# Kernel optimization log

Hardware: AMD Instinct MI355X
Metric: run time of the kernel (lower is better)

## Reference

```python
import jax, jax.numpy as jnp
import numpy as np

LMAX = 2
L = LMAX + 1          # number of l channels
M = (LMAX + 1) ** 2   # 9 spherical components
C = 64                # channels per l
N = 1024              # nodes
E = 300               # num_elements (hard-coded in module)
P3, P2, P1 = 16, 4, 2 # CG path counts for correlation 3/2/1


def so3_linear(x, w, b=None):
    # x: [N, M, Cin]; w: [L, Cout, Cin]. Per-l channel mixing (equivariant),
    # bias only on the l=0 (scalar) block.
    outs = []
    for l in range(L):
        seg = x[:, l * l:(l + 1) * (l + 1), :]
        y = jnp.einsum('nmc,dc->nmd', seg, w[l])
        if l == 0 and b is not None:
            y = y + b
        outs.append(y)
    return jnp.concatenate(outs, axis=1)


def setup_inputs() -> dict:
    key = jax.random.key(0)
    ks = jax.random.split(key, 13)
    s = lambda k, shape, sc=1.0: jax.random.normal(k, shape, dtype=jnp.float32) * sc
    return {
        'irreps_x': s(ks[0], (N, M, C)),
        'atomic_numbers': jax.random.randint(ks[1], (N,), 0, 119),
        'w_fc1': s(ks[2], (L, C, C), 1.0 / np.sqrt(C)),
        'b_fc1': jnp.zeros((C,), jnp.float32),
        'U3': s(ks[3], (M, M, M, M, P3), 0.05),   # generalized CG coeffs, corr 3
        'W3': s(ks[4], (E, P3, C), 1.0 / np.sqrt(P3 * C)),
        'U2': s(ks[5], (M, M, M, P2), 0.05),      # corr 2
        'W2': s(ks[6], (E, P2, C), 1.0 / np.sqrt(P2 * C)),
        'U1': s(ks[7], (M, M, P1), 0.05),         # corr 1
        'W1': s(ks[8], (E, P1, C), 1.0 / np.sqrt(P1 * C)),
        'w_lin': s(ks[9], (L, C, C), 1.0 / np.sqrt(C)),   # e3nn Linear in dtp block
        'w_fc2': s(ks[10], (L, C, C), 1.0 / np.sqrt(C)),  # final SO3_Linear
        'b_fc2': jnp.zeros((C,), jnp.float32),
    }


def reference(irreps_x, atomic_numbers, w_fc1, b_fc1, U3, W3, U2, W2, U1, W1,
              w_lin, w_fc2, b_fc2):
    # 1) irreps_small_fc
    x = so3_linear(irreps_x, w_fc1, b_fc1)           # [N, M, C]
    # 2) permute(0, 2, 1): MACE layout [N, C, M]
    xT = jnp.transpose(x, (0, 2, 1))
    # one_hot(atomic_numbers) @ W  ==  gather of per-element weights
    a = atomic_numbers.astype(jnp.int32)
    w3 = W3[a]                                        # [N, P3, C]
    w2 = W2[a]                                        # [N, P2, C]
    w1 = W1[a]                                        # [N, P1, C]
    # MACE symmetric contraction, correlation = 3:
    # out[n,c,o,a,b] = sum_{i,p} U3[o,a,b,i,p] * w3[n,p,c] * x[n,c,i]
    z = jnp.einsum('nci,npc->ncip', xT, w3)           # [N, C, M, P3]
    out = jnp.einsum('oabip,ncip->ncoab', U3, z)      # [N, C, M, M, M]
    # fold in correlation-2 term, contract one input index
    c2 = jnp.einsum('oaip,npc->ncoai', U2, w2)        # [N, C, M, M, M]
    out = jnp.einsum('ncoai,nci->ncoa', c2 + out, xT) # [N, C, M, M]
    # fold in correlation-1 term, contract last input index
    c1 = jnp.einsum('oip,npc->ncoi', U1, w1)          # [N, C, M, M]
    out = jnp.einsum('ncoi,nci->nco', c1 + out, xT)   # [N, C, M]
    # e3nn per-irrep Linear inside EquivariantProductBasisBlock (no bias)
    out = jnp.transpose(out, (0, 2, 1))               # back2orderTmul -> [N, M, C]
    out = so3_linear(out, w_lin)
    # 3) final SO3_Linear back to input channel count
    out = so3_linear(out, w_fc2, b_fc2)
    return out                                        # [N, M, C]
```

## Files before the change

### kernel.cpp

```cpp
#include <hip/hip_runtime.h>


typedef __attribute__((ext_vector_type(8)))  _Float16 f16x8;
typedef __attribute__((ext_vector_type(4)))  _Float16 f16x4;
typedef __attribute__((ext_vector_type(16))) float    f32x16;
typedef __attribute__((ext_vector_type(4)))  float    f32x4;
typedef __attribute__((ext_vector_type(8)))  short    short8;

static __device__ __forceinline__ unsigned short f2bf(float f) {
    union { float f; unsigned u; } v; v.f = f;
    unsigned r = v.u + 0x7fffu + ((v.u >> 16) & 1u);
    return (unsigned short)(r >> 16);
}

__global__ void prep_u3w(const float* __restrict__ U3, const float* __restrict__ U2,
                         _Float16* __restrict__ U3w)
{
    int idx = blockIdx.x * 256 + threadIdx.x;
    int ks = idx / 192, r = idx % 192;
    int nt = r >> 6, l = r & 63;
    int oa = nt * 32 + (l & 31), half = l >> 5;
    f16x8 v;
    if (ks < 81) {
        int b = ks / 9, ksub = ks % 9, ip0 = ksub * 16 + half * 8;
        #pragma unroll
        for (int j = 0; j < 8; ++j) {
            float f = (oa < 81) ? U3[(oa * 9 + b) * 144 + ip0 + j] : 0.f;
            v[j] = (_Float16)f;
        }
    } else {
        int ip0 = (ks - 81) * 16 + half * 8;
        #pragma unroll
        for (int j = 0; j < 8; ++j) {
            int ip2 = ip0 + j;
            float f = (oa < 81 && ip2 < 36) ? U2[oa * 36 + ip2] : 0.f;
            v[j] = (_Float16)f;
        }
    }
    ((f16x8*)U3w)[idx] = v;
}

__global__ __launch_bounds__(384, 3) void mace_main(
    const float* __restrict__ irreps_x,
    const int*   __restrict__ atomic_numbers,
    const float* __restrict__ w_fc1,
    const float* __restrict__ b_fc1,
    const float* __restrict__ W3,
    const float* __restrict__ W2,
    const float* __restrict__ U1,
    const float* __restrict__ W1,
    const float* __restrict__ w_lin,
    const float* __restrict__ w_fc2,
    const float* __restrict__ b_fc2,
    const _Float16* __restrict__ U3w,
    float* __restrict__ out)
{
    __shared__ float xvL[1152];
    __shared__ __align__(16) unsigned char region[47616];
    _Float16* const o2L       = (_Float16*)region;
    float* const o1L          = (float*)region;
    unsigned short* const XfA = (unsigned short*)(region + 4608);
    unsigned short* const WfA = (unsigned short*)(region + 17408);
    float* const yL           = (float*)(region + 43008);

    const int t  = threadIdx.x;
    const int n0 = blockIdx.x * 2;
    const int w  = t >> 6;
    const int l  = t & 63;
    const int kg = l >> 4;
    const int hf = l >> 5;
    const int c32 = l & 31;

    auto fill_Xf = [&](auto srcf) {
        for (int i = t; i < 32 * 96; i += 384) {
            int rr = i / 96, k = (i % 96) * 2;
            int lh = k >> 6, c = k & 63;
            float v0 = 0.f, v1 = 0.f;
            if (rr < 18) {
                int at = rr / 9, m = rr % 9;
                int lm = (m >= 4) ? 2 : (m >= 1 ? 1 : 0);
                if (lh == lm) { v0 = srcf(at, m, c); v1 = srcf(at, m, c + 1); }
            }
            unsigned pk = (unsigned)f2bf(v0) | ((unsigned)f2bf(v1) << 16);
            *(unsigned*)(XfA + rr * 200 + k) = pk;
        }
    };
    auto fill_Wf = [&](const float* wmat) {
        for (int i = t; i < 64 * 96; i += 384) {
            int d = i / 96, k = (i % 96) * 2;
            int lh = k >> 6, c = k & 63;
            const float* wp = wmat + lh * 4096 + d * 64 + c;
            unsigned pk = (unsigned)f2bf(wp[0]) | ((unsigned)f2bf(wp[1]) << 16);
            *(unsigned*)(WfA + d * 200 + k) = pk;
        }
    };
    auto run_linear = [&](const float* bias, float* dst, bool to_global) {
        for (int tile = w; tile < 8; tile += 6) {
            int rt = tile >> 2, ct = tile & 3;
            int row = rt * 16 + (l & 15);
            int col = ct * 16 + (l & 15);
            const unsigned short* ab = XfA + row * 200 + kg * 8;
            const unsigned short* bb = WfA + col * 200 + kg * 8;
            f32x4 acc0 = {0,0,0,0}, acc1 = {0,0,0,0};
            #pragma unroll
            for (int kt = 0; kt < 6; kt += 2) {
                short8 A0 = *(const short8*)(ab + kt * 32);
                short8 A1 = *(const short8*)(ab + (kt + 1) * 32);
                short8 B0 = *(const short8*)(bb + kt * 32);
                short8 B1 = *(const short8*)(bb + (kt + 1) * 32);
                acc0 = __builtin_amdgcn_mfma_f32_16x16x32_bf16(A0, B0, acc0, 0, 0, 0);
                acc1 = __builtin_amdgcn_mfma_f32_16x16x32_bf16(A1, B1, acc1, 0, 0, 0);
            }
            f32x4 acc = acc0 + acc1;
            #pragma unroll
            for (int r = 0; r < 4; ++r) {
                int rr = rt * 16 + kg * 4 + r;
                if (rr < 18) {
                    int at = rr / 9, m = rr % 9;
                    float v = acc[r];
                    if (bias && m == 0) v += bias[col];
                    if (to_global) dst[(n0 + at) * 576 + m * 64 + col] = v;
                    else           dst[at * 576 + m * 64 + col] = v;
                }
            }
        }
    };

    fill_Xf([&](int at, int m, int c) { return irreps_x[(n0 + at) * 576 + m * 64 + c]; });
    fill_Wf(w_fc1);
    __syncthreads();
    run_linear(b_fc1, xvL, false);
    __syncthreads();

    {
        const int at = w / 3, ng = w % 3;
        const int an = atomic_numbers[n0 + at];
        const float* xa  = xvL + at * 576;
        const float* W3r = W3 + an * 1024;
        const float* W2r = W2 + an * 256;

        f16x8 s3f[2][9];
        #pragma unroll
        for (int mt = 0; mt < 2; ++mt) {
            const int c = mt * 32 + c32;
            f16x8 w3h;
            #pragma unroll
            for (int j = 0; j < 8; ++j)
                w3h[j] = (_Float16)W3r[(hf * 8 + j) * 64 + c];
            #pragma unroll
            for (int i = 0; i < 9; ++i) {
                _Float16 xi = (_Float16)xa[i * 64 + c];
                f16x8 xi8 = {xi, xi, xi, xi, xi, xi, xi, xi};
                s3f[mt][i] = w3h * xi8;
            }
        }

        f32x16 acc0 = {0.f}, acc1 = {0.f};
        const f16x8* Bp = (const f16x8*)U3w + ng * 64 + l;
        for (int b = 0; b < 9; ++b) {
            _Float16 h0 = (_Float16)xa[b * 64 + c32];
            _Float16 h1 = (_Float16)xa[b * 64 + 32 + c32];
            f16x8 xb0 = {h0, h0, h0, h0, h0, h0, h0, h0};
            f16x8 xb1 = {h1, h1, h1, h1, h1, h1, h1, h1};
            const f16x8* Bb = Bp + b * 9 * 192;
            #pragma unroll
            for (int ksub = 0; ksub < 9; ++ksub) {
                f16x8 B = Bb[ksub * 192];
                acc0 = __builtin_amdgcn_mfma_f32_32x32x16_f16(s3f[0][ksub] * xb0, B, acc0, 0, 0, 0);
                acc1 = __builtin_amdgcn_mfma_f32_32x32x16_f16(s3f[1][ksub] * xb1, B, acc1, 0, 0, 0);
            }
        }
        #pragma unroll
        for (int ks2 = 0; ks2 < 3; ++ks2) {
            f16x8 a0, a1;
            #pragma unroll
            for (int j = 0; j < 8; ++j) {
                int ip2 = ks2 * 16 + hf * 8 + j;
                int ii = ip2 >> 2, pp = ip2 & 3;
                float f0 = 0.f, f1 = 0.f;
                if (ii < 9) {
                    f0 = xa[ii * 64 + c32]      * W2r[pp * 64 + c32];
                    f1 = xa[ii * 64 + 32 + c32] * W2r[pp * 64 + 32 + c32];
                }
                a0[j] = (_Float16)f0; a1[j] = (_Float16)f1;
            }
            f16x8 B = Bp[(81 + ks2) * 192];
            acc0 = __builtin_amdgcn_mfma_f32_32x32x16_f16(a0, B, acc0, 0, 0, 0);
            acc1 = __builtin_amdgcn_mfma_f32_32x32x16_f16(a1, B, acc1, 0, 0, 0);
        }

        const int oa = ng * 32 + c32;
        _Float16* o2row = o2L + (at * 96 + oa) * 68;
        #pragma unroll
        for (int q = 0; q < 4; ++q) {
            int c0 = q * 8 + hf * 4;
            f16x4 v0 = {(_Float16)acc0[q*4+0], (_Float16)acc0[q*4+1],
                        (_Float16)acc0[q*4+2], (_Float16)acc0[q*4+3]};
            f16x4 v1 = {(_Float16)acc1[q*4+0], (_Float16)acc1[q*4+1],
                        (_Float16)acc1[q*4+2], (_Float16)acc1[q*4+3]};
            *(f16x4*)(o2row + c0)      = v0;
            *(f16x4*)(o2row + 32 + c0) = v1;
        }
    }
    __syncthreads();

    float o1v[3];
    #pragma unroll
    for (int it = 0; it < 3; ++it) {
        int i = t + it * 384;
        int at2 = i / 576, r2 = i % 576, o = r2 >> 6, c = r2 & 63;
        int an2 = atomic_numbers[n0 + at2];
        float w1a = W1[an2 * 128 + c], w1b = W1[an2 * 128 + 64 + c];
        const _Float16* o2p = o2L + (at2 * 96 + o * 9) * 68 + c;
        float acc = 0.f, sa = 0.f, sb = 0.f;
        #pragma unroll
        for (int a = 0; a < 9; ++a)
            acc += (float)o2p[a * 68] * xvL[at2 * 576 + a * 64 + c];
        #pragma unroll
        for (int i2 = 0; i2 < 9; ++i2) {
            float xc = xvL[at2 * 576 + i2 * 64 + c];
            sa += U1[o * 18 + i2 * 2]     * xc;
            sb += U1[o * 18 + i2 * 2 + 1] * xc;
        }
        o1v[it] = acc + sa * w1a + sb * w1b;
    }
    __syncthreads();
    #pragma unroll
    for (int it = 0; it < 3; ++it) o1L[t + it * 384] = o1v[it];
    __syncthreads();

    fill_Xf([&](int at, int m, int c) { return o1L[at * 576 + m * 64 + c]; });
    fill_Wf(w_lin);
    __syncthreads();
    run_linear(nullptr, yL, false);
    __syncthreads();

    fill_Xf([&](int at, int m, int c) { return yL[at * 576 + m * 64 + c]; });
    fill_Wf(w_fc2);
    __syncthreads();
    run_linear(b_fc2, out, true);
}

extern "C" void kernel_launch(void* const* d_in, const int* in_sizes, int n_in,
                              void* d_out, int out_size, void* d_ws, size_t ws_size,
                              hipStream_t stream) {
    const float* irreps_x = (const float*)d_in[0];
    const int*   anum     = (const int*)d_in[1];
    const float* w_fc1    = (const float*)d_in[2];
    const float* b_fc1    = (const float*)d_in[3];
    const float* U3       = (const float*)d_in[4];
    const float* W3       = (const float*)d_in[5];
    const float* U2       = (const float*)d_in[6];
    const float* W2       = (const float*)d_in[7];
    const float* U1       = (const float*)d_in[8];
    const float* W1       = (const float*)d_in[9];
    const float* w_lin    = (const float*)d_in[10];
    const float* w_fc2    = (const float*)d_in[11];
    const float* b_fc2    = (const float*)d_in[12];
    float* out = (float*)d_out;

    _Float16* U3w = (_Float16*)d_ws;

    prep_u3w<<<63, 256, 0, stream>>>(U3, U2, U3w);
    mace_main<<<512, 384, 0, stream>>>(irreps_x, anum, w_fc1, b_fc1, W3, W2,
                                       U1, W1, w_lin, w_fc2, b_fc2, U3w, out);
}
```

Measured before the change: 140.8 us.

## Split fused kernel into linear/core kernels and pre-fold w_lin into w_fc2

Replaces the single fused per-two-node kernel with separate kernels: a scalar fp32 per-l linear for the first projection, a one-node-per-block core contraction kernel with higher occupancy, and a final linear that uses a precomputed product of w_fc2 and w_lin, so one of the three linears is removed. Intermediates round-trip through global memory (the output buffer and workspace), and the linears now run in fp32 FMA rather than bf16 MFMA. The risks are extra launches, extra global traffic, and a slower scalar linear path in exchange for more parallelism and less per-block serialization.

```diff
diff --git a/kernel.cpp b/kernel.cpp
--- a/kernel.cpp
+++ b/kernel.cpp
@@ -2,243 +2,168 @@
 
 
 typedef __attribute__((ext_vector_type(8)))  _Float16 f16x8;
-typedef __attribute__((ext_vector_type(4)))  _Float16 f16x4;
 typedef __attribute__((ext_vector_type(16))) float    f32x16;
 typedef __attribute__((ext_vector_type(4)))  float    f32x4;
-typedef __attribute__((ext_vector_type(8)))  short    short8;
 
-static __device__ __forceinline__ unsigned short f2bf(float f) {
-    union { float f; unsigned u; } v; v.f = f;
-    unsigned r = v.u + 0x7fffu + ((v.u >> 16) & 1u);
-    return (unsigned short)(r >> 16);
+__global__ void prep_misc(const float* __restrict__ U3, const float* __restrict__ U2,
+                          const float* __restrict__ w_lin, const float* __restrict__ w_fc2,
+                          _Float16* __restrict__ U3w, float* __restrict__ wcomb)
+{
+    if (blockIdx.x < 63) {
+        int idx = blockIdx.x * 256 + threadIdx.x;
+        int ks = idx / 192, r = idx % 192;
+        int nt = r >> 6, l = r & 63;
+        int oa = nt * 32 + (l & 31), half = l >> 5;
+        f16x8 v;
+        if (ks < 81) {
+            int b = ks / 9, ksub = ks % 9, ip0 = ksub * 16 + half * 8;
+            #pragma unroll
+            for (int j = 0; j < 8; ++j) {
+                float f = (oa < 81) ? U3[(oa * 9 + b) * 144 + ip0 + j] : 0.f;
+                v[j] = (_Float16)f;
+            }
+        } else {
+            int ip0 = (ks - 81) * 16 + half * 8;
+            #pragma unroll
+            for (int j = 0; j < 8; ++j) {
+                int ip2 = ip0 + j;
+                float f = (oa < 81 && ip2 < 36) ? U2[oa * 36 + ip2] : 0.f;
+                v[j] = (_Float16)f;
+            }
+        }
+        ((f16x8*)U3w)[idx] = v;
+    } else {
+        int l = blockIdx.x - 63;
+        const float* wf = w_fc2 + l * 4096;
+        const float* wl = w_lin + l * 4096;
+        for (int i = threadIdx.x; i < 4096; i += 256) {
+            int e = i >> 6, c = i & 63;
+            float s = 0.f;
+            #pragma unroll 8
+            for (int d = 0; d < 64; ++d) s += wf[e * 64 + d] * wl[d * 64 + c];
+            wcomb[l * 4096 + i] = s;
+        }
+    }
 }
 
-__global__ void prep_u3w(const float* __restrict__ U3, const float* __restrict__ U2,
-                         _Float16* __restrict__ U3w)
+__global__ __launch_bounds__(256) void lin_k(const float* __restrict__ x,
+                                             const float* __restrict__ w,
+                                             const float* __restrict__ bias,
+                                             float* __restrict__ y)
 {
-    int idx = blockIdx.x * 256 + threadIdx.x;
-    int ks = idx / 192, r = idx % 192;
-    int nt = r >> 6, l = r & 63;
-    int oa = nt * 32 + (l & 31), half = l >> 5;
-    f16x8 v;
-    if (ks < 81) {
-        int b = ks / 9, ksub = ks % 9, ip0 = ksub * 16 + half * 8;
-        #pragma unroll
-        for (int j = 0; j < 8; ++j) {
-            float f = (oa < 81) ? U3[(oa * 9 + b) * 144 + ip0 + j] : 0.f;
-            v[j] = (_Float16)f;
-        }
-    } else {
-        int ip0 = (ks - 81) * 16 + half * 8;
-        #pragma unroll
-        for (int j = 0; j < 8; ++j) {
-            int ip2 = ip0 + j;
-            float f = (oa < 81 && ip2 < 36) ? U2[oa * 36 + ip2] : 0.f;
-            v[j] = (_Float16)f;
-        }
+    __shared__ float xr[256];
+    const int nm0 = blockIdx.x * 4;
+    const int t = threadIdx.x;
+    xr[t] = x[nm0 * 64 + t];
+    __syncthreads();
+    const int r = t >> 6, d = t & 63;
+    const int m = (nm0 + r) % 9;
+    const int l = (m >= 4) ? 2 : (m >= 1 ? 1 : 0);
+    const float4* xv = (const float4*)(xr + r * 64);
+    const float4* wv = (const float4*)(w + l * 4096 + d * 64);
+    float acc = (m == 0) ? bias[d] : 0.f;
+    #pragma unroll
+    for (int q = 0; q < 16; ++q) {
+        float4 a = xv[q], b = wv[q];
+        acc += a.x * b.x + a.y * b.y + a.z * b.z + a.w * b.w;
     }
-    ((f16x8*)U3w)[idx] = v;
+    y[nm0 * 64 + t] = acc;
 }
 
-__global__ __launch_bounds__(384, 3) void mace_main(
-    const float* __restrict__ irreps_x,
-    const int*   __restrict__ atomic_numbers,
-    const float* __restrict__ w_fc1,
-    const float* __restrict__ b_fc1,
+__global__ __launch_bounds__(384, 6) void mace_core(
+    const float* __restrict__ xvg,
+    const int*   __restrict__ anum,
     const float* __restrict__ W3,
     const float* __restrict__ W2,
     const float* __restrict__ U1,
     const float* __restrict__ W1,
-    const float* __restrict__ w_lin,
-    const float* __restrict__ w_fc2,
-    const float* __restrict__ b_fc2,
     const _Float16* __restrict__ U3w,
-    float* __restrict__ out)
+    float* __restrict__ o1g)
 {
-    __shared__ float xvL[1152];
-    __shared__ __align__(16) unsigned char region[47616];
-    _Float16* const o2L       = (_Float16*)region;
-    float* const o1L          = (float*)region;
-    unsigned short* const XfA = (unsigned short*)(region + 4608);
-    unsigned short* const WfA = (unsigned short*)(region + 17408);
-    float* const yL           = (float*)(region + 43008);
+    __shared__ float xvL[576];
+    __shared__ __align__(16) float o2L[96 * 68];
 
+    const int n  = blockIdx.x;
     const int t  = threadIdx.x;
-    const int n0 = blockIdx.x * 2;
     const int w  = t >> 6;
     const int l  = t & 63;
-    const int kg = l >> 4;
-    const int hf = l >> 5;
-    const int c32 = l & 31;
+    const int mt = w & 1, ng = w >> 1;
+    const int c32 = l & 31, hf = l >> 5;
+    const int c  = mt * 32 + c32;
 
-    auto fill_Xf = [&](auto srcf) {
-        for (int i = t; i < 32 * 96; i += 384) {
-            int rr = i / 96, k = (i % 96) * 2;
-            int lh = k >> 6, c = k & 63;
-            float v0 = 0.f, v1 = 0.f;
-            if (rr < 18) {
-                int at = rr / 9, m = rr % 9;
-                int lm = (m >= 4) ? 2 : (m >= 1 ? 1 : 0);
-                if (lh == lm) { v0 = srcf(at, m, c); v1 = srcf(at, m, c + 1); }
-            }
-            unsigned pk = (unsigned)f2bf(v0) | ((unsigned)f2bf(v1) << 16);
-            *(unsigned*)(XfA + rr * 200 + k) = pk;
-        }
-    };
-    auto fill_Wf = [&](const float* wmat) {
-        for (int i = t; i < 64 * 96; i += 384) {
-            int d = i / 96, k = (i % 96) * 2;
-            int lh = k >> 6, c = k & 63;
-            const float* wp = wmat + lh * 4096 + d * 64 + c;
-            unsigned pk = (unsigned)f2bf(wp[0]) | ((unsigned)f2bf(wp[1]) << 16);
-            *(unsigned*)(WfA + d * 200 + k) = pk;
-        }
-    };
-    auto run_linear = [&](const float* bias, float* dst, bool to_global) {
-        for (int tile = w; tile < 8; tile += 6) {
-            int rt = tile >> 2, ct = tile & 3;
-            int row = rt * 16 + (l & 15);
-            int col = ct * 16 + (l & 15);
-            const unsigned short* ab = XfA + row * 200 + kg * 8;
-            const unsigned short* bb = WfA + col * 200 + kg * 8;
-            f32x4 acc0 = {0,0,0,0}, acc1 = {0,0,0,0};
-            #pragma unroll
-            for (int kt = 0; kt < 6; kt += 2) {
-                short8 A0 = *(const short8*)(ab + kt * 32);
-                short8 A1 = *(const short8*)(ab + (kt + 1) * 32);
-                short8 B0 = *(const short8*)(bb + kt * 32);
-                short8 B1 = *(const short8*)(bb + (kt + 1) * 32);
-                acc0 = __builtin_amdgcn_mfma_f32_16x16x32_bf16(A0, B0, acc0, 0, 0, 0);
-                acc1 = __builtin_amdgcn_mfma_f32_16x16x32_bf16(A1, B1, acc1, 0, 0, 0);
-            }
-            f32x4 acc = acc0 + acc1;
-            #pragma unroll
-            for (int r = 0; r < 4; ++r) {
-                int rr = rt * 16 + kg * 4 + r;
-                if (rr < 18) {
-                    int at = rr / 9, m = rr % 9;
-                    float v = acc[r];
-                    if (bias && m == 0) v += bias[col];
-                    if (to_global) dst[(n0 + at) * 576 + m * 64 + col] = v;
-                    else           dst[at * 576 + m * 64 + col] = v;
-                }
-            }
-        }
-    };
-
-    fill_Xf([&](int at, int m, int c) { return irreps_x[(n0 + at) * 576 + m * 64 + c]; });
-    fill_Wf(w_fc1);
-    __syncthreads();
-    run_linear(b_fc1, xvL, false);
+    for (int i = t; i < 576; i += 384) xvL[i] = xvg[n * 576 + i];
     __syncthreads();
 
+    const int an = anum[n];
+    const float* W3r = W3 + an * 1024;
+    const float* W2r = W2 + an * 256;
+
+    f16x8 s3f[9];
     {
-        const int at = w / 3, ng = w % 3;
-        const int an = atomic_numbers[n0 + at];
-        const float* xa  = xvL + at * 576;
-        const float* W3r = W3 + an * 1024;
-        const float* W2r = W2 + an * 256;
+        f16x8 w3h;
+        #pragma unroll
+        for (int j = 0; j < 8; ++j)
+            w3h[j] = (_Float16)W3r[(hf * 8 + j) * 64 + c];
+        #pragma unroll
+        for (int i = 0; i < 9; ++i) {
+            _Float16 xi = (_Float16)xvL[i * 64 + c];
+            f16x8 xi8 = {xi, xi, xi, xi, xi, xi, xi, xi};
+            s3f[i] = w3h * xi8;
+        }
+    }
 
-        f16x8 s3f[2][9];
+    f32x16 acc = {0.f};
+    const f16x8* Bp = (const f16x8*)U3w + ng * 64 + l;
+    for (int b = 0; b < 9; ++b) {
+        _Float16 h = (_Float16)xvL[b * 64 + c];
+        f16x8 xb = {h, h, h, h, h, h, h, h};
+        const f16x8* Bb = Bp + b * 9 * 192;
         #pragma unroll
-        for (int mt = 0; mt < 2; ++mt) {
-            const int c = mt * 32 + c32;
-            f16x8 w3h;
-            #pragma unroll
-            for (int j = 0; j < 8; ++j)
-                w3h[j] = (_Float16)W3r[(hf * 8 + j) * 64 + c];
-            #pragma unroll
-            for (int i = 0; i < 9; ++i) {
-                _Float16 xi = (_Float16)xa[i * 64 + c];
-                f16x8 xi8 = {xi, xi, xi, xi, xi, xi, xi, xi};
-                s3f[mt][i] = w3h * xi8;
-            }
+        for (int ksub = 0; ksub < 9; ++ksub)
+            acc = __builtin_amdgcn_mfma_f32_32x32x16_f16(s3f[ksub] * xb, Bb[ksub * 192], acc, 0, 0, 0);
+    }
+    #pragma unroll
+    for (int ks2 = 0; ks2 < 3; ++ks2) {
+        f16x8 a;
+        #pragma unroll
+        for (int j = 0; j < 8; ++j) {
+            int ip2 = ks2 * 16 + hf * 8 + j;
+            int ii = ip2 >> 2, pp = ip2 & 3;
+            float f = (ii < 9) ? xvL[ii * 64 + c] * W2r[pp * 64 + c] : 0.f;
+            a[j] = (_Float16)f;
         }
+        acc = __builtin_amdgcn_mfma_f32_32x32x16_f16(a, Bp[(81 + ks2) * 192], acc, 0, 0, 0);
+    }
 
-        f32x16 acc0 = {0.f}, acc1 = {0.f};
-        const f16x8* Bp = (const f16x8*)U3w + ng * 64 + l;
-        for (int b = 0; b < 9; ++b) {
-            _Float16 h0 = (_Float16)xa[b * 64 + c32];
-            _Float16 h1 = (_Float16)xa[b * 64 + 32 + c32];
-            f16x8 xb0 = {h0, h0, h0, h0, h0, h0, h0, h0};
-            f16x8 xb1 = {h1, h1, h1, h1, h1, h1, h1, h1};
-            const f16x8* Bb = Bp + b * 9 * 192;
-            #pragma unroll
-            for (int ksub = 0; ksub < 9; ++ksub) {
-                f16x8 B = Bb[ksub * 192];
-                acc0 = __builtin_amdgcn_mfma_f32_32x32x16_f16(s3f[0][ksub] * xb0, B, acc0, 0, 0, 0);
-                acc1 = __builtin_amdgcn_mfma_f32_32x32x16_f16(s3f[1][ksub] * xb1, B, acc1, 0, 0, 0);
-            }
-        }
-        #pragma unroll
-        for (int ks2 = 0; ks2 < 3; ++ks2) {
-            f16x8 a0, a1;
-            #pragma unroll
-            for (int j = 0; j < 8; ++j) {
-                int ip2 = ks2 * 16 + hf * 8 + j;
-                int ii = ip2 >> 2, pp = ip2 & 3;
-                float f0 = 0.f, f1 = 0.f;
-                if (ii < 9) {
-                    f0 = xa[ii * 64 + c32]      * W2r[pp * 64 + c32];
-                    f1 = xa[ii * 64 + 32 + c32] * W2r[pp * 64 + 32 + c32];
-                }
-                a0[j] = (_Float16)f0; a1[j] = (_Float16)f1;
-            }
-            f16x8 B = Bp[(81 + ks2) * 192];
-            acc0 = __builtin_amdgcn_mfma_f32_32x32x16_f16(a0, B, acc0, 0, 0, 0);
-            acc1 = __builtin_amdgcn_mfma_f32_32x32x16_f16(a1, B, acc1, 0, 0, 0);
-        }
-
+    {
         const int oa = ng * 32 + c32;
-        _Float16* o2row = o2L + (at * 96 + oa) * 68;
+        float* o2row = o2L + oa * 68 + mt * 32;
         #pragma unroll
         for (int q = 0; q < 4; ++q) {
-            int c0 = q * 8 + hf * 4;
-            f16x4 v0 = {(_Float16)acc0[q*4+0], (_Float16)acc0[q*4+1],
-                        (_Float16)acc0[q*4+2], (_Float16)acc0[q*4+3]};
-            f16x4 v1 = {(_Float16)acc1[q*4+0], (_Float16)acc1[q*4+1],
-                        (_Float16)acc1[q*4+2], (_Float16)acc1[q*4+3]};
-            *(f16x4*)(o2row + c0)      = v0;
-            *(f16x4*)(o2row + 32 + c0) = v1;
+            f32x4 v = {acc[q*4+0], acc[q*4+1], acc[q*4+2], acc[q*4+3]};
+            *(f32x4*)(o2row + q * 8 + hf * 4) = v;
         }
     }
     __syncthreads();
 
-    float o1v[3];
     #pragma unroll
-    for (int it = 0; it < 3; ++it) {
-        int i = t + it * 384;
-        int at2 = i / 576, r2 = i % 576, o = r2 >> 6, c = r2 & 63;
-        int an2 = atomic_numbers[n0 + at2];
-        float w1a = W1[an2 * 128 + c], w1b = W1[an2 * 128 + 64 + c];
-        const _Float16* o2p = o2L + (at2 * 96 + o * 9) * 68 + c;
-        float acc = 0.f, sa = 0.f, sb = 0.f;
-        #pragma unroll
-        for (int a = 0; a < 9; ++a)
-            acc += (float)o2p[a * 68] * xvL[at2 * 576 + a * 64 + c];
-        #pragma unroll
-        for (int i2 = 0; i2 < 9; ++i2) {
-            float xc = xvL[at2 * 576 + i2 * 64 + c];
-            sa += U1[o * 18 + i2 * 2]     * xc;
-            sb += U1[o * 18 + i2 * 2 + 1] * xc;
+    for (int it = 0; it < 2; ++it) {
+        int idx = t + it * 384;
+        if (idx < 576) {
+            int o = idx >> 6, cc = idx & 63;
+            float a1 = 0.f, sa = 0.f, sb = 0.f;
+            #pragma unroll
+            for (int a = 0; a < 9; ++a)
+                a1 += o2L[(o * 9 + a) * 68 + cc] * xvL[a * 64 + cc];
+            #pragma unroll
+            for (int i2 = 0; i2 < 9; ++i2) {
+                float xc = xvL[i2 * 64 + cc];
+                sa += U1[o * 18 + i2 * 2]     * xc;
+                sb += U1[o * 18 + i2 * 2 + 1] * xc;
+            }
+            o1g[n * 576 + idx] = a1 + sa * W1[an * 128 + cc] + sb * W1[an * 128 + 64 + cc];
         }
-        o1v[it] = acc + sa * w1a + sb * w1b;
     }
-    __syncthreads();
-    #pragma unroll
-    for (int it = 0; it < 3; ++it) o1L[t + it * 384] = o1v[it];
-    __syncthreads();
-
-    fill_Xf([&](int at, int m, int c) { return o1L[at * 576 + m * 64 + c]; });
-    fill_Wf(w_lin);
-    __syncthreads();
-    run_linear(nullptr, yL, false);
-    __syncthreads();
-
-    fill_Xf([&](int at, int m, int c) { return yL[at * 576 + m * 64 + c]; });
-    fill_Wf(w_fc2);
-    __syncthreads();
-    run_linear(b_fc2, out, true);
 }
 
 extern "C" void kernel_launch(void* const* d_in, const int* in_sizes, int n_in,
@@ -259,9 +184,13 @@
     const float* b_fc2    = (const float*)d_in[12];
     float* out = (float*)d_out;
 
-    _Float16* U3w = (_Float16*)d_ws;
+    _Float16* U3w  = (_Float16*)d_ws;
+    float*    o1g  = (float*)((char*)d_ws + 258048);
+    float*    wcomb= (float*)((char*)d_ws + 258048 + 2359296);
+    float*    xvg  = out;
 
-    prep_u3w<<<63, 256, 0, stream>>>(U3, U2, U3w);
-    mace_main<<<512, 384, 0, stream>>>(irreps_x, anum, w_fc1, b_fc1, W3, W2,
-                                       U1, W1, w_lin, w_fc2, b_fc2, U3w, out);
+    prep_misc<<<66, 256, 0, stream>>>(U3, U2, w_lin, w_fc2, U3w, wcomb);
+    lin_k<<<2304, 256, 0, stream>>>(irreps_x, w_fc1, b_fc1, xvg);
+    mace_core<<<1024, 384, 0, stream>>>(xvg, anum, W3, W2, U1, W1, U3w, o1g);
+    lin_k<<<2304, 256, 0, stream>>>(o1g, wcomb, b_fc2, out);
 }
```

New measurement: 175.6 us. 24.7% more time.
